# Kernel tuning notes

Hardware: AMD Instinct MI355X
Metric: run time of the kernel (lower is better)

Reference implementation:

```python
import jax, jax.numpy as jnp
import numpy as np

B = 128
K = 16
# (in_ch, featdim, dim) per stage, matching conv1..conv11
DIMS = [(3, 8, 2048), (8, 32, 1024), (32, 64, 512), (64, 64, 256), (64, 64, 128),
        (64, 128, 64), (128, 256, 32), (256, 512, 16), (512, 512, 8), (512, 512, 4),
        (512, 1024, 2)]


def setup_inputs() -> dict:
    key = jax.random.key(0)
    ks = jax.random.split(key, 64)
    inp = {"x": jax.random.normal(ks[0], (B, 3, 2048), dtype=jnp.float32)}
    i = 1
    for li, (cin, cf, d) in enumerate(DIMS, start=1):
        inp[f"W{li}"] = jax.random.normal(ks[i], (3 * cf, cin), dtype=jnp.float32) / np.sqrt(cin).astype(np.float32); i += 1
        inp[f"b{li}"] = jax.random.normal(ks[i], (3 * cf,), dtype=jnp.float32) * 0.01; i += 1
        inp[f"sel{li}"] = jax.random.randint(ks[i], (d,), 0, 3); i += 1
    inp["fcW"] = jax.random.normal(ks[i], (K, 1024), dtype=jnp.float32) / np.sqrt(1024).astype(np.float32); i += 1
    inp["fcb"] = jax.random.normal(ks[i], (K,), dtype=jnp.float32) * 0.01
    return inp


def kdconv(x, W, b, sel, featdim, dim):
    # 1x1 conv == per-position matmul: x [B, Cin, dim] -> y [B, 3*featdim, dim]
    y = jax.nn.relu(jnp.einsum('oi,bin->bon', W, x) + b[None, :, None])
    y = y.reshape(-1, featdim, 3, dim)
    # kd split-dim gather: pick one of the 3 feature groups per position
    y = jnp.take_along_axis(y, sel[None, None, None, :], axis=2)[:, :, 0, :]  # [B, featdim, dim]
    # pairwise max-pool of sibling leaves
    return y.reshape(-1, featdim, dim // 2, 2).max(axis=-1)  # [B, featdim, dim//2]


def reference(x, sel1, sel2, sel3, sel4, sel5, sel6, sel7, sel8, sel9, sel10, sel11,
              W1, b1, W2, b2, W3, b3, W4, b4, W5, b5, W6, b6, W7, b7, W8, b8,
              W9, b9, W10, b10, W11, b11, fcW, fcb):
    Ws = [W1, W2, W3, W4, W5, W6, W7, W8, W9, W10, W11]
    bs = [b1, b2, b3, b4, b5, b6, b7, b8, b9, b10, b11]
    sels = [sel1, sel2, sel3, sel4, sel5, sel6, sel7, sel8, sel9, sel10, sel11]
    h = x
    for (cin, cf, d), W, b, s in zip(DIMS, Ws, bs, sels):
        h = kdconv(h, W, b, s, cf, d)
    h = h.reshape(-1, 1024)  # [B, 1024]
    return jax.nn.log_softmax(h @ fcW.T + fcb, axis=-1)
```

## Files before the change

### kernel.cpp

```cpp
#include <hip/hip_runtime.h>
#include <math.h>

typedef __attribute__((ext_vector_type(8))) short bf16x8;
typedef __attribute__((ext_vector_type(4))) float f32x4;

__device__ __forceinline__ unsigned short f2bf(float f) {
    unsigned u = __builtin_bit_cast(unsigned, f);
    u += 0x7FFF + ((u >> 16) & 1);
    return (unsigned short)(u >> 16);
}
__device__ __forceinline__ float bf2f(unsigned short h) {
    unsigned u = ((unsigned)h) << 16;
    return __builtin_bit_cast(float, u);
}

#define O_W3 0
#define O_W4 6144
#define O_W5 18432
#define O_W6 30720
#define O_W7 55296
#define O_W8 153600
#define O_W9 546816
#define O_W10 1333248
#define O_W11 2119680

template<int CIN>
__device__ __forceinline__ void mfma_tile(
    const unsigned short* a0, const unsigned short* a1,
    const unsigned short* b0p, const unsigned short* b1p,
    f32x4& acc0, f32x4& acc1)
{
#pragma unroll
    for (int k = 0; k < CIN; k += 32) {
        bf16x8 A0 = __builtin_bit_cast(bf16x8, *(const float4*)(const void*)(a0 + k));
        bf16x8 A1 = __builtin_bit_cast(bf16x8, *(const float4*)(const void*)(a1 + k));
        bf16x8 B0 = __builtin_bit_cast(bf16x8, *(const float4*)(const void*)(b0p + k));
        bf16x8 B1 = __builtin_bit_cast(bf16x8, *(const float4*)(const void*)(b1p + k));
        acc0 = __builtin_amdgcn_mfma_f32_16x16x32_bf16(A0, B0, acc0, 0, 0, 0);
        acc1 = __builtin_amdgcn_mfma_f32_16x16x32_bf16(A1, B1, acc1, 0, 0, 0);
    }
}

__device__ __forceinline__ void epilogue_store(
    unsigned short* dst, const f32x4& acc0, const f32x4& acc1,
    const float* bias, int fbase, int s0, int s1)
{
    unsigned short o[4];
#pragma unroll
    for (int r = 0; r < 4; ++r) {
        float v = fmaxf(fmaxf(acc0[r] + bias[(fbase + r) * 3 + s0],
                              acc1[r] + bias[(fbase + r) * 3 + s1]), 0.f);
        o[r] = f2bf(v);
    }
    *(ushort4*)dst = make_ushort4(o[0], o[1], o[2], o[3]);
}

struct PackParams { const float* Wsrc[9]; unsigned short* Wb; };

__global__ __launch_bounds__(256) void pack_w_kernel(PackParams P)
{
    int gt = blockIdx.x * 256 + threadIdx.x;
    const int we[9] = {6144, 12288, 12288, 24576, 98304, 393216, 786432, 786432, 1572864};
    int off = 0;
#pragma unroll
    for (int li = 0; li < 9; ++li) {
        const float4* src = (const float4*)P.Wsrc[li];
        ushort4* dst = (ushort4*)(P.Wb + off);
        int n4 = we[li] >> 2;
        for (int i = gt; i < n4; i += 65536) {
            float4 w = src[i];
            dst[i] = make_ushort4(f2bf(w.x), f2bf(w.y), f2bf(w.z), f2bf(w.w));
        }
        off += we[li];
    }
}

struct FusedParams {
    const float* x;
    const float* W1; const float* B1; const int* S1;
    const float* W2; const float* B2; const int* S2;
    const float* Bl[9];
    const int*   Sl[9];
    const unsigned short* Wb;
    unsigned short* X8;
};

#define A_XS   0
#define A_L1O  25344
#define A_WSM  41728
#define A_L2O  45568
#define A_L3O  0
#define A_L4O  45568
#define A_L5O  0
#define A_L6O  45568
#define ARENA_BYTES 86528

__global__ __launch_bounds__(512) void fused17_kernel(FusedParams P)
{
    __shared__ __align__(16) char arena[ARENA_BYTES];

    const int tid  = threadIdx.x;
    const int bg   = blockIdx.x >> 4;
    const int sl   = blockIdx.x & 15;
    const int lane = tid & 63;
    const int wv   = tid >> 6;
    const int c    = lane & 15, q = lane >> 4;

    const unsigned short* W3b = P.Wb + O_W3;
    const unsigned short* W4b = P.Wb + O_W4;
    const unsigned short* W5b = P.Wb + O_W5;
    const unsigned short* W6b = P.Wb + O_W6;
    const unsigned short* W7b = P.Wb + O_W7;

    {
        float* xsf = (float*)(arena + A_XS);
        const float* xg = P.x + (size_t)(bg * 16) * 6144 + sl * 128;
        for (int i = tid; i < 6144; i += 512) {
            int b = i / 384;
            int r = i - b * 384;
            int cc = r >> 7, p = r & 127;
            xsf[b * 396 + cc * 132 + p] = xg[(size_t)b * 6144 + cc * 2048 + p];
        }
        float* wsm = (float*)(arena + A_WSM);
        for (int i = tid; i < 960; i += 512) {
            float v;
            if (i < 72)       v = P.W1[i];
            else if (i < 96)  v = P.B1[i - 72];
            else if (i < 864) v = P.W2[i - 96];
            else              v = P.B2[i - 864];
            wsm[i] = v;
        }
    }
    __syncthreads();

    {
        const float* xsf = (const float*)(arena + A_XS);
        const float* wl1 = (const float*)(arena + A_WSM);
        const float* bl1 = wl1 + 72;
        unsigned short* L1o = (unsigned short*)(arena + A_L1O);
        for (int i = tid; i < 1024; i += 512) {
            int n = i >> 4, b = i & 15;
            int np1 = sl * 64 + n;
            int s0 = P.S1[2 * np1], s1 = P.S1[2 * np1 + 1];
            const float* xb0 = xsf + b * 396 + 2 * n;
            float c0x = xb0[0],   c0y = xb0[1];
            float c1x = xb0[132], c1y = xb0[133];
            float c2x = xb0[264], c2y = xb0[265];
            unsigned short o[8];
#pragma unroll
            for (int f = 0; f < 8; ++f) {
                int r0 = f * 3 + s0, r1 = f * 3 + s1;
                float z0 = fmaf(wl1[r0*3+2], c2x, fmaf(wl1[r0*3+1], c1x, fmaf(wl1[r0*3+0], c0x, bl1[r0])));
                float z1 = fmaf(wl1[r1*3+2], c2y, fmaf(wl1[r1*3+1], c1y, fmaf(wl1[r1*3+0], c0y, bl1[r1])));
                o[f] = f2bf(fmaxf(fmaxf(z0, z1), 0.f));
            }
            unsigned short* dst = L1o + (n * 16 + b) * 8;
            *(ushort4*)dst       = make_ushort4(o[0], o[1], o[2], o[3]);
            *(ushort4*)(dst + 4) = make_ushort4(o[4], o[5], o[6], o[7]);
        }
    }
    __syncthreads();

    {
        const float* wl2 = (const float*)(arena + A_WSM) + 96;
        const float* bl2 = (const float*)(arena + A_WSM) + 864;
        const unsigned short* L1o = (const unsigned short*)(arena + A_L1O);
        unsigned short* L2o = (unsigned short*)(arena + A_L2O);
        {
            int i = tid;
            int n = i >> 4, b = i & 15;
            int np2 = sl * 32 + n;
            int s0 = P.S2[2 * np2], s1 = P.S2[2 * np2 + 1];
            const unsigned short* r0 = L1o + ((2 * n) * 16 + b) * 8;
            const unsigned short* r1 = L1o + ((2 * n + 1) * 16 + b) * 8;
            float xa[8], xb2[8];
            {
                ushort4 u0 = *(const ushort4*)r0, u1 = *(const ushort4*)(r0 + 4);
                ushort4 v0 = *(const ushort4*)r1, v1 = *(const ushort4*)(r1 + 4);
                xa[0]=bf2f(u0.x); xa[1]=bf2f(u0.y); xa[2]=bf2f(u0.z); xa[3]=bf2f(u0.w);
                xa[4]=bf2f(u1.x); xa[5]=bf2f(u1.y); xa[6]=bf2f(u1.z); xa[7]=bf2f(u1.w);
                xb2[0]=bf2f(v0.x); xb2[1]=bf2f(v0.y); xb2[2]=bf2f(v0.z); xb2[3]=bf2f(v0.w);
                xb2[4]=bf2f(v1.x); xb2[5]=bf2f(v1.y); xb2[6]=bf2f(v1.z); xb2[7]=bf2f(v1.w);
            }
            unsigned short o[32];
#pragma unroll
            for (int f = 0; f < 32; ++f) {
                const float* w0 = &wl2[(f * 3 + s0) * 8];
                const float* w1 = &wl2[(f * 3 + s1) * 8];
                float z0 = bl2[f * 3 + s0], z1 = bl2[f * 3 + s1];
#pragma unroll
                for (int k = 0; k < 8; ++k) {
                    z0 = fmaf(w0[k], xa[k], z0);
                    z1 = fmaf(w1[k], xb2[k], z1);
                }
                o[f] = f2bf(fmaxf(fmaxf(z0, z1), 0.f));
            }
            unsigned short* dst = L2o + (n * 16 + b) * 40;
#pragma unroll
            for (int i2 = 0; i2 < 8; ++i2)
                *(ushort4*)(dst + 4 * i2) = make_ushort4(o[4*i2], o[4*i2+1], o[4*i2+2], o[4*i2+3]);
        }
    }
    __syncthreads();

    {
        const unsigned short* L2o = (const unsigned short*)(arena + A_L2O);
        unsigned short* L3o = (unsigned short*)(arena + A_L3O);
        const int* S3 = P.Sl[0]; const float* B3 = P.Bl[0];
#pragma unroll 2
        for (int t = wv; t < 64; t += 8) {
            int n3 = t >> 2, ft = t & 3;
            int np = sl * 16 + n3;
            int s0 = __builtin_amdgcn_readfirstlane(S3[2 * np]);
            int s1 = __builtin_amdgcn_readfirstlane(S3[2 * np + 1]);
            int f0 = ft * 16;
            const unsigned short* a0 = W3b + ((f0 + c) * 3 + s0) * 32 + q * 8;
            const unsigned short* a1 = W3b + ((f0 + c) * 3 + s1) * 32 + q * 8;
            const unsigned short* bp0 = L2o + ((2 * n3) * 16 + c) * 40 + q * 8;
            const unsigned short* bp1 = L2o + ((2 * n3 + 1) * 16 + c) * 40 + q * 8;
            f32x4 acc0 = {0.f,0.f,0.f,0.f}, acc1 = {0.f,0.f,0.f,0.f};
            mfma_tile<32>(a0, a1, bp0, bp1, acc0, acc1);
            epilogue_store(L3o + (n3 * 16 + c) * 72 + f0 + q * 4,
                           acc0, acc1, B3, f0 + q * 4, s0, s1);
        }
    }
    __syncthreads();

    {
        const unsigned short* L3o = (const unsigned short*)(arena + A_L3O);
        unsigned short* L4o = (unsigned short*)(arena + A_L4O);
        const int* S4 = P.Sl[1]; const float* B4 = P.Bl[1];
#pragma unroll 2
        for (int t = wv; t < 32; t += 8) {
            int n4 = t >> 2, ft = t & 3;
            int np = sl * 8 + n4;
            int s0 = __builtin_amdgcn_readfirstlane(S4[2 * np]);
            int s1 = __builtin_amdgcn_readfirstlane(S4[2 * np + 1]);
            int f0 = ft * 16;
            const unsigned short* a0 = W4b + ((f0 + c) * 3 + s0) * 64 + q * 8;
            const unsigned short* a1 = W4b + ((f0 + c) * 3 + s1) * 64 + q * 8;
            const unsigned short* bp0 = L3o + ((2 * n4) * 16 + c) * 72 + q * 8;
            const unsigned short* bp1 = L3o + ((2 * n4 + 1) * 16 + c) * 72 + q * 8;
            f32x4 acc0 = {0.f,0.f,0.f,0.f}, acc1 = {0.f,0.f,0.f,0.f};
            mfma_tile<64>(a0, a1, bp0, bp1, acc0, acc1);
            epilogue_store(L4o + (n4 * 16 + c) * 72 + f0 + q * 4,
                           acc0, acc1, B4, f0 + q * 4, s0, s1);
        }
    }
    __syncthreads();

    {
        const unsigned short* L4o = (const unsigned short*)(arena + A_L4O);
        unsigned short* L5o = (unsigned short*)(arena + A_L5O);
        const int* S5 = P.Sl[2]; const float* B5 = P.Bl[2];
        for (int t = wv; t < 16; t += 8) {
            int n5 = t >> 2, ft = t & 3;
            int np = sl * 4 + n5;
            int s0 = __builtin_amdgcn_readfirstlane(S5[2 * np]);
            int s1 = __builtin_amdgcn_readfirstlane(S5[2 * np + 1]);
            int f0 = ft * 16;
            const unsigned short* a0 = W5b + ((f0 + c) * 3 + s0) * 64 + q * 8;
            const unsigned short* a1 = W5b + ((f0 + c) * 3 + s1) * 64 + q * 8;
            const unsigned short* bp0 = L4o + ((2 * n5) * 16 + c) * 72 + q * 8;
            const unsigned short* bp1 = L4o + ((2 * n5 + 1) * 16 + c) * 72 + q * 8;
            f32x4 acc0 = {0.f,0.f,0.f,0.f}, acc1 = {0.f,0.f,0.f,0.f};
            mfma_tile<64>(a0, a1, bp0, bp1, acc0, acc1);
            epilogue_store(L5o + (n5 * 16 + c) * 72 + f0 + q * 4,
                           acc0, acc1, B5, f0 + q * 4, s0, s1);
        }
    }
    __syncthreads();

    {
        const unsigned short* L5o = (const unsigned short*)(arena + A_L5O);
        unsigned short* L6o = (unsigned short*)(arena + A_L6O);
        const int* S6 = P.Sl[3]; const float* B6 = P.Bl[3];
        for (int t = wv; t < 16; t += 8) {
            int n6 = t >> 3, ft = t & 7;
            int np = sl * 2 + n6;
            int s0 = __builtin_amdgcn_readfirstlane(S6[2 * np]);
            int s1 = __builtin_amdgcn_readfirstlane(S6[2 * np + 1]);
            int f0 = ft * 16;
            const unsigned short* a0 = W6b + ((f0 + c) * 3 + s0) * 64 + q * 8;
            const unsigned short* a1 = W6b + ((f0 + c) * 3 + s1) * 64 + q * 8;
            const unsigned short* bp0 = L5o + ((2 * n6) * 16 + c) * 72 + q * 8;
            const unsigned short* bp1 = L5o + ((2 * n6 + 1) * 16 + c) * 72 + q * 8;
            f32x4 acc0 = {0.f,0.f,0.f,0.f}, acc1 = {0.f,0.f,0.f,0.f};
            mfma_tile<64>(a0, a1, bp0, bp1, acc0, acc1);
            epilogue_store(L6o + (n6 * 16 + c) * 136 + f0 + q * 4,
                           acc0, acc1, B6, f0 + q * 4, s0, s1);
        }
    }
    __syncthreads();

    {
        const unsigned short* L6o = (const unsigned short*)(arena + A_L6O);
        const int* S7 = P.Sl[4]; const float* B7 = P.Bl[4];
        int s0 = __builtin_amdgcn_readfirstlane(S7[2 * sl]);
        int s1 = __builtin_amdgcn_readfirstlane(S7[2 * sl + 1]);
#pragma unroll 2
        for (int t = wv; t < 16; t += 8) {
            int f0 = t * 16;
            const unsigned short* a0 = W7b + (size_t)((f0 + c) * 3 + s0) * 128 + q * 8;
            const unsigned short* a1 = W7b + (size_t)((f0 + c) * 3 + s1) * 128 + q * 8;
            const unsigned short* bp0 = L6o + (0 * 16 + c) * 136 + q * 8;
            const unsigned short* bp1 = L6o + (1 * 16 + c) * 136 + q * 8;
            f32x4 acc0 = {0.f,0.f,0.f,0.f}, acc1 = {0.f,0.f,0.f,0.f};
            mfma_tile<128>(a0, a1, bp0, bp1, acc0, acc1);
            epilogue_store(P.X8 + ((size_t)sl * 128 + bg * 16 + c) * 256 + f0 + q * 4,
                           acc0, acc1, B7, f0 + q * 4, s0, s1);
        }
    }
}

template<int CIN, int CF, int NP, int MW, int NW>
__global__ __launch_bounds__(256) void mfma_kernel(
    const unsigned short* __restrict__ Xin,
    const unsigned short* __restrict__ Wb,
    const float* __restrict__ bias,
    const int*   __restrict__ sel,
    unsigned short* __restrict__ Xout)
{
    constexpr int FT = CF / (16 * MW);
    constexpr int BT = 128 / (16 * NW);

    const int wid  = threadIdx.x >> 6;
    const int lane = threadIdx.x & 63;
    const int task = blockIdx.x * 4 + wid;
    const int bi = task % BT;
    const int fi = (task / BT) % FT;
    const int n  = task / (BT * FT);

    const int c = lane & 15;
    const int q = lane >> 4;
    const int s0 = __builtin_amdgcn_readfirstlane(sel[2 * n]);
    const int s1 = __builtin_amdgcn_readfirstlane(sel[2 * n + 1]);

    const int f0 = fi * 16 * MW;
    const int b0 = bi * 16 * NW;

    const unsigned short* ap[2][MW];
    const unsigned short* bp[2][NW];
#pragma unroll
    for (int p = 0; p < 2; ++p) {
        int s = p ? s1 : s0;
#pragma unroll
        for (int mi = 0; mi < MW; ++mi)
            ap[p][mi] = Wb + (size_t)((f0 + mi * 16 + c) * 3 + s) * CIN + q * 8;
#pragma unroll
        for (int ni = 0; ni < NW; ++ni)
            bp[p][ni] = Xin + ((size_t)(2 * n + p) * 128 + b0 + ni * 16 + c) * CIN + q * 8;
    }

    f32x4 acc[2][MW][NW];
#pragma unroll
    for (int p = 0; p < 2; ++p)
#pragma unroll
        for (int mi = 0; mi < MW; ++mi)
#pragma unroll
            for (int ni = 0; ni < NW; ++ni)
                acc[p][mi][ni] = (f32x4){0.f, 0.f, 0.f, 0.f};

#pragma unroll 2
    for (int k = 0; k < CIN; k += 32) {
        bf16x8 A[2][MW], B[2][NW];
#pragma unroll
        for (int p = 0; p < 2; ++p) {
#pragma unroll
            for (int mi = 0; mi < MW; ++mi)
                A[p][mi] = __builtin_bit_cast(bf16x8, *(const float4*)(const void*)(ap[p][mi] + k));
#pragma unroll
            for (int ni = 0; ni < NW; ++ni)
                B[p][ni] = __builtin_bit_cast(bf16x8, *(const float4*)(const void*)(bp[p][ni] + k));
        }
#pragma unroll
        for (int p = 0; p < 2; ++p)
#pragma unroll
            for (int mi = 0; mi < MW; ++mi)
#pragma unroll
                for (int ni = 0; ni < NW; ++ni)
                    acc[p][mi][ni] = __builtin_amdgcn_mfma_f32_16x16x32_bf16(
                        A[p][mi], B[p][ni], acc[p][mi][ni], 0, 0, 0);
    }

#pragma unroll
    for (int mi = 0; mi < MW; ++mi) {
        int fbase = f0 + mi * 16 + q * 4;
#pragma unroll
        for (int ni = 0; ni < NW; ++ni) {
            int b = b0 + ni * 16 + c;
            epilogue_store(Xout + ((size_t)n * 128 + b) * CF + fbase,
                           acc[0][mi][ni], acc[1][mi][ni], bias, fbase, s0, s1);
        }
    }
}

__global__ __launch_bounds__(256) void fc_logsoftmax_kernel(
    const unsigned short* __restrict__ h, const float* __restrict__ fcW,
    const float* __restrict__ fcb, float* __restrict__ out)
{
    int b   = blockIdx.x;
    int tid = threadIdx.x;
    int k     = tid & 15;
    int chunk = tid >> 4;

    const float* __restrict__ wk = fcW + (size_t)k * 1024;
    const unsigned short* hb = h + (size_t)b * 1024;

    float partial = 0.0f;
    int j0 = chunk * 64;
#pragma unroll 8
    for (int j = 0; j < 64; ++j)
        partial = fmaf(bf2f(hb[j0 + j]), wk[j0 + j], partial);

    __shared__ float red[16][17];
    red[chunk][k] = partial;
    __syncthreads();

    __shared__ float logits[16];
    if (tid < 16) {
        float s = fcb[tid];
#pragma unroll
        for (int c = 0; c < 16; ++c) s += red[c][tid];
        logits[tid] = s;
    }
    __syncthreads();

    if (tid < 16) {
        float mx = -INFINITY;
#pragma unroll
        for (int kk = 0; kk < 16; ++kk) mx = fmaxf(mx, logits[kk]);
        float se = 0.0f;
#pragma unroll
        for (int kk = 0; kk < 16; ++kk) se += expf(logits[kk] - mx);
        out[b * 16 + tid] = logits[tid] - mx - logf(se);
    }
}

extern "C" void kernel_launch(void* const* d_in, const int* in_sizes, int n_in,
                              void* d_out, int out_size, void* d_ws, size_t ws_size,
                              hipStream_t stream)
{
#define WL(i) (const float*)d_in[1 + 3 * (i)]
#define BL(i) (const float*)d_in[2 + 3 * (i)]
#define SL(i) (const int*)  d_in[3 + 3 * (i)]

    unsigned short* bufA = (unsigned short*)d_ws;
    unsigned short* bufB = bufA + 2u * 1024u * 1024u;
    unsigned short* Wb   = bufB + 2u * 1024u * 1024u;

    PackParams PP;
    for (int i = 0; i < 9; ++i) PP.Wsrc[i] = WL(2 + i);
    PP.Wb = Wb;
    pack_w_kernel<<<256, 256, 0, stream>>>(PP);

    FusedParams FP;
    FP.x  = (const float*)d_in[0];
    FP.W1 = WL(0); FP.B1 = BL(0); FP.S1 = SL(0);
    FP.W2 = WL(1); FP.B2 = BL(1); FP.S2 = SL(1);
    for (int i = 0; i < 9; ++i) {
        FP.Bl[i] = BL(2 + i);
        FP.Sl[i] = SL(2 + i);
    }
    FP.Wb = Wb; FP.X8 = bufA;
    fused17_kernel<<<128, 512, 0, stream>>>(FP);

    mfma_kernel<256, 512, 8, 2, 2><<<128, 256, 0, stream>>>(bufA, Wb + O_W8,  BL(7),  SL(7),  bufB);
    mfma_kernel<512, 512, 4, 1, 1><<<256, 256, 0, stream>>>(bufB, Wb + O_W9,  BL(8),  SL(8),  bufA);
    mfma_kernel<512, 512, 2, 1, 1><<<128, 256, 0, stream>>>(bufA, Wb + O_W10, BL(9),  SL(9),  bufB);
    mfma_kernel<512, 1024, 1, 1, 1><<<128, 256, 0, stream>>>(bufB, Wb + O_W11, BL(10), SL(10), bufA);

    fc_logsoftmax_kernel<<<128, 256, 0, stream>>>(bufA, (const float*)d_in[34], (const float*)d_in[35], (float*)d_out);

#undef WL
#undef BL
#undef SL
}
```

Baseline: 211.6 us.

## Fold weight packing into fused kernel and read early-layer weights as fp32

Removes the separate pack_w kernel launch. Extra blocks of the fused layer-1..7 kernel now convert the W8–W11 weights to bf16, running alongside the 128 compute blocks. Layers 3–7 read fp32 weights directly and convert them in registers instead of waiting for packed copies. The fused kernel also grows to 1024 threads per block, stages selection indices and biases in shared memory, and drops its per-stage loops. This saves a launch and a serialization point, at the cost of redundant per-block fp32→bf16 conversion and twice the weight bytes read for layers 3–7.

```diff
diff --git a/kernel.cpp b/kernel.cpp
--- a/kernel.cpp
+++ b/kernel.cpp
@@ -14,26 +14,32 @@
     return __builtin_bit_cast(float, u);
 }
 
-#define O_W3 0
-#define O_W4 6144
-#define O_W5 18432
-#define O_W6 30720
-#define O_W7 55296
 #define O_W8 153600
 #define O_W9 546816
 #define O_W10 1333248
 #define O_W11 2119680
 
+__device__ __forceinline__ bf16x8 ldcvt8(const float* p) {
+    float4 u0 = *(const float4*)p;
+    float4 u1 = *(const float4*)(p + 4);
+    bf16x8 r;
+    r[0] = (short)f2bf(u0.x); r[1] = (short)f2bf(u0.y);
+    r[2] = (short)f2bf(u0.z); r[3] = (short)f2bf(u0.w);
+    r[4] = (short)f2bf(u1.x); r[5] = (short)f2bf(u1.y);
+    r[6] = (short)f2bf(u1.z); r[7] = (short)f2bf(u1.w);
+    return r;
+}
+
 template<int CIN>
-__device__ __forceinline__ void mfma_tile(
-    const unsigned short* a0, const unsigned short* a1,
+__device__ __forceinline__ void mfma_tile_f32A(
+    const float* a0f, const float* a1f,
     const unsigned short* b0p, const unsigned short* b1p,
     f32x4& acc0, f32x4& acc1)
 {
 #pragma unroll
     for (int k = 0; k < CIN; k += 32) {
-        bf16x8 A0 = __builtin_bit_cast(bf16x8, *(const float4*)(const void*)(a0 + k));
-        bf16x8 A1 = __builtin_bit_cast(bf16x8, *(const float4*)(const void*)(a1 + k));
+        bf16x8 A0 = ldcvt8(a0f + k);
+        bf16x8 A1 = ldcvt8(a1f + k);
         bf16x8 B0 = __builtin_bit_cast(bf16x8, *(const float4*)(const void*)(b0p + k));
         bf16x8 B1 = __builtin_bit_cast(bf16x8, *(const float4*)(const void*)(b1p + k));
         acc0 = __builtin_amdgcn_mfma_f32_16x16x32_bf16(A0, B0, acc0, 0, 0, 0);
@@ -55,80 +61,105 @@
     *(ushort4*)dst = make_ushort4(o[0], o[1], o[2], o[3]);
 }
 
-struct PackParams { const float* Wsrc[9]; unsigned short* Wb; };
-
-__global__ __launch_bounds__(256) void pack_w_kernel(PackParams P)
-{
-    int gt = blockIdx.x * 256 + threadIdx.x;
-    const int we[9] = {6144, 12288, 12288, 24576, 98304, 393216, 786432, 786432, 1572864};
-    int off = 0;
-#pragma unroll
-    for (int li = 0; li < 9; ++li) {
-        const float4* src = (const float4*)P.Wsrc[li];
-        ushort4* dst = (ushort4*)(P.Wb + off);
-        int n4 = we[li] >> 2;
-        for (int i = gt; i < n4; i += 65536) {
-            float4 w = src[i];
-            dst[i] = make_ushort4(f2bf(w.x), f2bf(w.y), f2bf(w.z), f2bf(w.w));
-        }
-        off += we[li];
-    }
-}
-
 struct FusedParams {
     const float* x;
     const float* W1; const float* B1; const int* S1;
     const float* W2; const float* B2; const int* S2;
+    const float* Wsrc[9];
     const float* Bl[9];
     const int*   Sl[9];
-    const unsigned short* Wb;
+    unsigned short* Wb;
     unsigned short* X8;
 };
 
-#define A_XS   0
-#define A_L1O  25344
-#define A_WSM  41728
-#define A_L2O  45568
-#define A_L3O  0
-#define A_L4O  45568
-#define A_L5O  0
-#define A_L6O  45568
-#define ARENA_BYTES 86528
-
-__global__ __launch_bounds__(512) void fused17_kernel(FusedParams P)
-{
+#define A_SELB 0
+#define A_XS   8192
+#define A_L1O  33536
+#define A_WSM  49920
+#define A_L2O  53760
+#define A_L3O  8192
+#define A_L4O  53760
+#define A_L5O  8192
+#define A_L6O  53760
+#define ARENA_BYTES 94720
+
+__global__ __launch_bounds__(1024) void fused17_kernel(FusedParams P)
+{
+    const int tid = threadIdx.x;
+
+    if (blockIdx.x >= 128) {
+        int gt = (blockIdx.x - 128) * 1024 + tid;
+        const int we[4] = {393216, 786432, 786432, 1572864};
+        const int wo[4] = {O_W8, O_W9, O_W10, O_W11};
+#pragma unroll
+        for (int li = 0; li < 4; ++li) {
+            const float4* src = (const float4*)P.Wsrc[5 + li];
+            ushort4* dst = (ushort4*)(P.Wb + wo[li]);
+            int n4 = we[li] >> 2;
+            for (int i = gt; i < n4; i += 65536) {
+                float4 w = src[i];
+                dst[i] = make_ushort4(f2bf(w.x), f2bf(w.y), f2bf(w.z), f2bf(w.w));
+            }
+        }
+        return;
+    }
+
     __shared__ __align__(16) char arena[ARENA_BYTES];
 
-    const int tid  = threadIdx.x;
     const int bg   = blockIdx.x >> 4;
     const int sl   = blockIdx.x & 15;
     const int lane = tid & 63;
     const int wv   = tid >> 6;
     const int c    = lane & 15, q = lane >> 4;
 
-    const unsigned short* W3b = P.Wb + O_W3;
-    const unsigned short* W4b = P.Wb + O_W4;
-    const unsigned short* W5b = P.Wb + O_W5;
-    const unsigned short* W6b = P.Wb + O_W6;
-    const unsigned short* W7b = P.Wb + O_W7;
+    int*   si  = (int*)(arena + A_SELB);
+    float* bfs = (float*)(arena + A_SELB + 1024);
+    const int* S1L = si;
+    const int* S2L = si + 128;
+    const int* S3L = si + 192;
+    const int* S4L = si + 224;
+    const int* S5L = si + 240;
+    const int* S6L = si + 248;
+    const int* S7L = si + 252;
+    const float* B3L = bfs;
+    const float* B4L = bfs + 192;
+    const float* B5L = bfs + 384;
+    const float* B6L = bfs + 576;
+    const float* B7L = bfs + 960;
 
     {
         float* xsf = (float*)(arena + A_XS);
         const float* xg = P.x + (size_t)(bg * 16) * 6144 + sl * 128;
-        for (int i = tid; i < 6144; i += 512) {
+        for (int i = tid; i < 6144; i += 1024) {
             int b = i / 384;
             int r = i - b * 384;
             int cc = r >> 7, p = r & 127;
             xsf[b * 396 + cc * 132 + p] = xg[(size_t)b * 6144 + cc * 2048 + p];
         }
         float* wsm = (float*)(arena + A_WSM);
-        for (int i = tid; i < 960; i += 512) {
+        if (tid < 960) {
             float v;
-            if (i < 72)       v = P.W1[i];
-            else if (i < 96)  v = P.B1[i - 72];
-            else if (i < 864) v = P.W2[i - 96];
-            else              v = P.B2[i - 864];
-            wsm[i] = v;
+            if (tid < 72)       v = P.W1[tid];
+            else if (tid < 96)  v = P.B1[tid - 72];
+            else if (tid < 864) v = P.W2[tid - 96];
+            else                v = P.B2[tid - 864];
+            wsm[tid] = v;
+        }
+        if (tid < 128)      si[tid] = P.S1[sl * 128 + tid];
+        else if (tid < 192) si[tid] = P.S2[sl * 64 + (tid - 128)];
+        else if (tid < 224) si[tid] = P.Sl[0][sl * 32 + (tid - 192)];
+        else if (tid < 240) si[tid] = P.Sl[1][sl * 16 + (tid - 224)];
+        else if (tid < 248) si[tid] = P.Sl[2][sl * 8  + (tid - 240)];
+        else if (tid < 252) si[tid] = P.Sl[3][sl * 4  + (tid - 248)];
+        else if (tid < 254) si[tid] = P.Sl[4][sl * 2  + (tid - 252)];
+        for (int i = tid; i < 1728; i += 1024) {
+            float v;
+            if (i < 192)      v = P.Bl[0][i];
+            else if (i < 384) v = P.Bl[1][i - 192];
+            else if (i < 576) v = P.Bl[2][i - 384];
+            else if (i < 960) v = P.Bl[3][i - 576];
+            else              v = P.Bl[4][i - 960];
+            bfs[i] = v;
         }
     }
     __syncthreads();
@@ -138,26 +169,23 @@
         const float* wl1 = (const float*)(arena + A_WSM);
         const float* bl1 = wl1 + 72;
         unsigned short* L1o = (unsigned short*)(arena + A_L1O);
-        for (int i = tid; i < 1024; i += 512) {
-            int n = i >> 4, b = i & 15;
-            int np1 = sl * 64 + n;
-            int s0 = P.S1[2 * np1], s1 = P.S1[2 * np1 + 1];
-            const float* xb0 = xsf + b * 396 + 2 * n;
-            float c0x = xb0[0],   c0y = xb0[1];
-            float c1x = xb0[132], c1y = xb0[133];
-            float c2x = xb0[264], c2y = xb0[265];
-            unsigned short o[8];
-#pragma unroll
-            for (int f = 0; f < 8; ++f) {
-                int r0 = f * 3 + s0, r1 = f * 3 + s1;
-                float z0 = fmaf(wl1[r0*3+2], c2x, fmaf(wl1[r0*3+1], c1x, fmaf(wl1[r0*3+0], c0x, bl1[r0])));
-                float z1 = fmaf(wl1[r1*3+2], c2y, fmaf(wl1[r1*3+1], c1y, fmaf(wl1[r1*3+0], c0y, bl1[r1])));
-                o[f] = f2bf(fmaxf(fmaxf(z0, z1), 0.f));
-            }
-            unsigned short* dst = L1o + (n * 16 + b) * 8;
-            *(ushort4*)dst       = make_ushort4(o[0], o[1], o[2], o[3]);
-            *(ushort4*)(dst + 4) = make_ushort4(o[4], o[5], o[6], o[7]);
-        }
+        int n = tid >> 4, b = tid & 15;
+        int s0 = S1L[2 * n], s1 = S1L[2 * n + 1];
+        const float* xb0 = xsf + b * 396 + 2 * n;
+        float c0x = xb0[0],   c0y = xb0[1];
+        float c1x = xb0[132], c1y = xb0[133];
+        float c2x = xb0[264], c2y = xb0[265];
+        unsigned short o[8];
+#pragma unroll
+        for (int f = 0; f < 8; ++f) {
+            int r0 = f * 3 + s0, r1 = f * 3 + s1;
+            float z0 = fmaf(wl1[r0*3+2], c2x, fmaf(wl1[r0*3+1], c1x, fmaf(wl1[r0*3+0], c0x, bl1[r0])));
+            float z1 = fmaf(wl1[r1*3+2], c2y, fmaf(wl1[r1*3+1], c1y, fmaf(wl1[r1*3+0], c0y, bl1[r1])));
+            o[f] = f2bf(fmaxf(fmaxf(z0, z1), 0.f));
+        }
+        unsigned short* dst = L1o + (n * 16 + b) * 8;
+        *(ushort4*)dst       = make_ushort4(o[0], o[1], o[2], o[3]);
+        *(ushort4*)(dst + 4) = make_ushort4(o[4], o[5], o[6], o[7]);
     }
     __syncthreads();
 
@@ -166,62 +194,58 @@
         const float* bl2 = (const float*)(arena + A_WSM) + 864;
         const unsigned short* L1o = (const unsigned short*)(arena + A_L1O);
         unsigned short* L2o = (unsigned short*)(arena + A_L2O);
+        int n = tid >> 5, b = (tid >> 1) & 15, fh = tid & 1;
+        int s0 = S2L[2 * n], s1 = S2L[2 * n + 1];
+        const unsigned short* r0 = L1o + ((2 * n) * 16 + b) * 8;
+        const unsigned short* r1 = L1o + ((2 * n + 1) * 16 + b) * 8;
+        float xa[8], xb2[8];
         {
-            int i = tid;
-            int n = i >> 4, b = i & 15;
-            int np2 = sl * 32 + n;
-            int s0 = P.S2[2 * np2], s1 = P.S2[2 * np2 + 1];
-            const unsigned short* r0 = L1o + ((2 * n) * 16 + b) * 8;
-            const unsigned short* r1 = L1o + ((2 * n + 1) * 16 + b) * 8;
-            float xa[8], xb2[8];
-            {
-                ushort4 u0 = *(const ushort4*)r0, u1 = *(const ushort4*)(r0 + 4);
-                ushort4 v0 = *(const ushort4*)r1, v1 = *(const ushort4*)(r1 + 4);
-                xa[0]=bf2f(u0.x); xa[1]=bf2f(u0.y); xa[2]=bf2f(u0.z); xa[3]=bf2f(u0.w);
-                xa[4]=bf2f(u1.x); xa[5]=bf2f(u1.y); xa[6]=bf2f(u1.z); xa[7]=bf2f(u1.w);
-                xb2[0]=bf2f(v0.x); xb2[1]=bf2f(v0.y); xb2[2]=bf2f(v0.z); xb2[3]=bf2f(v0.w);
-                xb2[4]=bf2f(v1.x); xb2[5]=bf2f(v1.y); xb2[6]=bf2f(v1.z); xb2[7]=bf2f(v1.w);
+            ushort4 u0 = *(const ushort4*)r0, u1 = *(const ushort4*)(r0 + 4);
+            ushort4 v0 = *(const ushort4*)r1, v1 = *(const ushort4*)(r1 + 4);
+            xa[0]=bf2f(u0.x); xa[1]=bf2f(u0.y); xa[2]=bf2f(u0.z); xa[3]=bf2f(u0.w);
+            xa[4]=bf2f(u1.x); xa[5]=bf2f(u1.y); xa[6]=bf2f(u1.z); xa[7]=bf2f(u1.w);
+            xb2[0]=bf2f(v0.x); xb2[1]=bf2f(v0.y); xb2[2]=bf2f(v0.z); xb2[3]=bf2f(v0.w);
+            xb2[4]=bf2f(v1.x); xb2[5]=bf2f(v1.y); xb2[6]=bf2f(v1.z); xb2[7]=bf2f(v1.w);
+        }
+        unsigned short o[16];
+#pragma unroll
+        for (int fl = 0; fl < 16; ++fl) {
+            int f = fh * 16 + fl;
+            const float* w0 = &wl2[(f * 3 + s0) * 8];
+            const float* w1 = &wl2[(f * 3 + s1) * 8];
+            float z0 = bl2[f * 3 + s0], z1 = bl2[f * 3 + s1];
+#pragma unroll
+            for (int k = 0; k < 8; ++k) {
+                z0 = fmaf(w0[k], xa[k], z0);
+                z1 = fmaf(w1[k], xb2[k], z1);
             }
-            unsigned short o[32];
-#pragma unroll
-            for (int f = 0; f < 32; ++f) {
-                const float* w0 = &wl2[(f * 3 + s0) * 8];
-                const float* w1 = &wl2[(f * 3 + s1) * 8];
-                float z0 = bl2[f * 3 + s0], z1 = bl2[f * 3 + s1];
-#pragma unroll
-                for (int k = 0; k < 8; ++k) {
-                    z0 = fmaf(w0[k], xa[k], z0);
-                    z1 = fmaf(w1[k], xb2[k], z1);
-                }
-                o[f] = f2bf(fmaxf(fmaxf(z0, z1), 0.f));
-            }
-            unsigned short* dst = L2o + (n * 16 + b) * 40;
-#pragma unroll
-            for (int i2 = 0; i2 < 8; ++i2)
-                *(ushort4*)(dst + 4 * i2) = make_ushort4(o[4*i2], o[4*i2+1], o[4*i2+2], o[4*i2+3]);
-        }
+            o[fl] = f2bf(fmaxf(fmaxf(z0, z1), 0.f));
+        }
+        unsigned short* dst = L2o + (n * 16 + b) * 40 + fh * 16;
+#pragma unroll
+        for (int i2 = 0; i2 < 4; ++i2)
+            *(ushort4*)(dst + 4 * i2) = make_ushort4(o[4*i2], o[4*i2+1], o[4*i2+2], o[4*i2+3]);
     }
     __syncthreads();
 
     {
         const unsigned short* L2o = (const unsigned short*)(arena + A_L2O);
         unsigned short* L3o = (unsigned short*)(arena + A_L3O);
-        const int* S3 = P.Sl[0]; const float* B3 = P.Bl[0];
+        const float* W3f = P.Wsrc[0];
 #pragma unroll 2
-        for (int t = wv; t < 64; t += 8) {
+        for (int t = wv; t < 64; t += 16) {
             int n3 = t >> 2, ft = t & 3;
-            int np = sl * 16 + n3;
-            int s0 = __builtin_amdgcn_readfirstlane(S3[2 * np]);
-            int s1 = __builtin_amdgcn_readfirstlane(S3[2 * np + 1]);
+            int s0 = __builtin_amdgcn_readfirstlane(S3L[2 * n3]);
+            int s1 = __builtin_amdgcn_readfirstlane(S3L[2 * n3 + 1]);
             int f0 = ft * 16;
-            const unsigned short* a0 = W3b + ((f0 + c) * 3 + s0) * 32 + q * 8;
-            const unsigned short* a1 = W3b + ((f0 + c) * 3 + s1) * 32 + q * 8;
+            const float* a0f = W3f + ((f0 + c) * 3 + s0) * 32 + q * 8;
+            const float* a1f = W3f + ((f0 + c) * 3 + s1) * 32 + q * 8;
             const unsigned short* bp0 = L2o + ((2 * n3) * 16 + c) * 40 + q * 8;
             const unsigned short* bp1 = L2o + ((2 * n3 + 1) * 16 + c) * 40 + q * 8;
             f32x4 acc0 = {0.f,0.f,0.f,0.f}, acc1 = {0.f,0.f,0.f,0.f};
-            mfma_tile<32>(a0, a1, bp0, bp1, acc0, acc1);
+            mfma_tile_f32A<32>(a0f, a1f, bp0, bp1, acc0, acc1);
             epilogue_store(L3o + (n3 * 16 + c) * 72 + f0 + q * 4,
-                           acc0, acc1, B3, f0 + q * 4, s0, s1);
+                           acc0, acc1, B3L, f0 + q * 4, s0, s1);
         }
     }
     __syncthreads();
@@ -229,22 +253,21 @@
     {
         const unsigned short* L3o = (const unsigned short*)(arena + A_L3O);
         unsigned short* L4o = (unsigned short*)(arena + A_L4O);
-        const int* S4 = P.Sl[1]; const float* B4 = P.Bl[1];
-#pragma unroll 2
-        for (int t = wv; t < 32; t += 8) {
+        const float* W4f = P.Wsrc[1];
+#pragma unroll
+        for (int t = wv; t < 32; t += 16) {
             int n4 = t >> 2, ft = t & 3;
-            int np = sl * 8 + n4;
-            int s0 = __builtin_amdgcn_readfirstlane(S4[2 * np]);
-            int s1 = __builtin_amdgcn_readfirstlane(S4[2 * np + 1]);
+            int s0 = __builtin_amdgcn_readfirstlane(S4L[2 * n4]);
+            int s1 = __builtin_amdgcn_readfirstlane(S4L[2 * n4 + 1]);
             int f0 = ft * 16;
-            const unsigned short* a0 = W4b + ((f0 + c) * 3 + s0) * 64 + q * 8;
-            const unsigned short* a1 = W4b + ((f0 + c) * 3 + s1) * 64 + q * 8;
+            const float* a0f = W4f + ((f0 + c) * 3 + s0) * 64 + q * 8;
+            const float* a1f = W4f + ((f0 + c) * 3 + s1) * 64 + q * 8;
             const unsigned short* bp0 = L3o + ((2 * n4) * 16 + c) * 72 + q * 8;
             const unsigned short* bp1 = L3o + ((2 * n4 + 1) * 16 + c) * 72 + q * 8;
             f32x4 acc0 = {0.f,0.f,0.f,0.f}, acc1 = {0.f,0.f,0.f,0.f};
-            mfma_tile<64>(a0, a1, bp0, bp1, acc0, acc1);
+            mfma_tile_f32A<64>(a0f, a1f, bp0, bp1, acc0, acc1);
             epilogue_store(L4o + (n4 * 16 + c) * 72 + f0 + q * 4,
-                           acc0, acc1, B4, f0 + q * 4, s0, s1);
+                           acc0, acc1, B4L, f0 + q * 4, s0, s1);
         }
     }
     __syncthreads();
@@ -252,64 +275,57 @@
     {
         const unsigned short* L4o = (const unsigned short*)(arena + A_L4O);
         unsigned short* L5o = (unsigned short*)(arena + A_L5O);
-        const int* S5 = P.Sl[2]; const float* B5 = P.Bl[2];
-        for (int t = wv; t < 16; t += 8) {
-            int n5 = t >> 2, ft = t & 3;
-            int np = sl * 4 + n5;
-            int s0 = __builtin_amdgcn_readfirstlane(S5[2 * np]);
-            int s1 = __builtin_amdgcn_readfirstlane(S5[2 * np + 1]);
-            int f0 = ft * 16;
-            const unsigned short* a0 = W5b + ((f0 + c) * 3 + s0) * 64 + q * 8;
-            const unsigned short* a1 = W5b + ((f0 + c) * 3 + s1) * 64 + q * 8;
-            const unsigned short* bp0 = L4o + ((2 * n5) * 16 + c) * 72 + q * 8;
-            const unsigned short* bp1 = L4o + ((2 * n5 + 1) * 16 + c) * 72 + q * 8;
-            f32x4 acc0 = {0.f,0.f,0.f,0.f}, acc1 = {0.f,0.f,0.f,0.f};
-            mfma_tile<64>(a0, a1, bp0, bp1, acc0, acc1);
-            epilogue_store(L5o + (n5 * 16 + c) * 72 + f0 + q * 4,
-                           acc0, acc1, B5, f0 + q * 4, s0, s1);
-        }
+        const float* W5f = P.Wsrc[2];
+        int t = wv;
+        int n5 = t >> 2, ft = t & 3;
+        int s0 = __builtin_amdgcn_readfirstlane(S5L[2 * n5]);
+        int s1 = __builtin_amdgcn_readfirstlane(S5L[2 * n5 + 1]);
+        int f0 = ft * 16;
+        const float* a0f = W5f + ((f0 + c) * 3 + s0) * 64 + q * 8;
+        const float* a1f = W5f + ((f0 + c) * 3 + s1) * 64 + q * 8;
+        const unsigned short* bp0 = L4o + ((2 * n5) * 16 + c) * 72 + q * 8;
+        const unsigned short* bp1 = L4o + ((2 * n5 + 1) * 16 + c) * 72 + q * 8;
+        f32x4 acc0 = {0.f,0.f,0.f,0.f}, acc1 = {0.f,0.f,0.f,0.f};
+        mfma_tile_f32A<64>(a0f, a1f, bp0, bp1, acc0, acc1);
+        epilogue_store(L5o + (n5 * 16 + c) * 72 + f0 + q * 4,
+                       acc0, acc1, B5L, f0 + q * 4, s0, s1);
     }
     __syncthreads();
 
     {
         const unsigned short* L5o = (const unsigned short*)(arena + A_L5O);
         unsigned short* L6o = (unsigned short*)(arena + A_L6O);
-        const int* S6 = P.Sl[3]; const float* B6 = P.Bl[3];
-        for (int t = wv; t < 16; t += 8) {
-            int n6 = t >> 3, ft = t & 7;
-            int np = sl * 2 + n6;
-            int s0 = __builtin_amdgcn_readfirstlane(S6[2 * np]);
-            int s1 = __builtin_amdgcn_readfirstlane(S6[2 * np + 1]);
-            int f0 = ft * 16;
-            const unsigned short* a0 = W6b + ((f0 + c) * 3 + s0) * 64 + q * 8;
-            const unsigned short* a1 = W6b + ((f0 + c) * 3 + s1) * 64 + q * 8;
-            const unsigned short* bp0 = L5o + ((2 * n6) * 16 + c) * 72 + q * 8;
-            const unsigned short* bp1 = L5o + ((2 * n6 + 1) * 16 + c) * 72 + q * 8;
-            f32x4 acc0 = {0.f,0.f,0.f,0.f}, acc1 = {0.f,0.f,0.f,0.f};
-            mfma_tile<64>(a0, a1, bp0, bp1, acc0, acc1);
-            epilogue_store(L6o + (n6 * 16 + c) * 136 + f0 + q * 4,
-                           acc0, acc1, B6, f0 + q * 4, s0, s1);
-        }
+        const float* W6f = P.Wsrc[3];
+        int t = wv;
+        int n6 = t >> 3, ft = t & 7;
+        int s0 = __builtin_amdgcn_readfirstlane(S6L[2 * n6]);
+        int s1 = __builtin_amdgcn_readfirstlane(S6L[2 * n6 + 1]);
+        int f0 = ft * 16;
+        const float* a0f = W6f + ((f0 + c) * 3 + s0) * 64 + q * 8;
+        const float* a1f = W6f + ((f0 + c) * 3 + s1) * 64 + q * 8;
+        const unsigned short* bp0 = L5o + ((2 * n6) * 16 + c) * 72 + q * 8;
+        const unsigned short* bp1 = L5o + ((2 * n6 + 1) * 16 + c) * 72 + q * 8;
+        f32x4 acc0 = {0.f,0.f,0.f,0.f}, acc1 = {0.f,0.f,0.f,0.f};
+        mfma_tile_f32A<64>(a0f, a1f, bp0, bp1, acc0, acc1);
+        epilogue_store(L6o + (n6 * 16 + c) * 136 + f0 + q * 4,
+                       acc0, acc1, B6L, f0 + q * 4, s0, s1);
     }
     __syncthreads();
 
     {
         const unsigned short* L6o = (const unsigned short*)(arena + A_L6O);
-        const int* S7 = P.Sl[4]; const float* B7 = P.Bl[4];
-        int s0 = __builtin_amdgcn_readfirstlane(S7[2 * sl]);
-        int s1 = __builtin_amdgcn_readfirstlane(S7[2 * sl + 1]);
-#pragma unroll 2
-        for (int t = wv; t < 16; t += 8) {
-            int f0 = t * 16;
-            const unsigned short* a0 = W7b + (size_t)((f0 + c) * 3 + s0) * 128 + q * 8;
-            const unsigned short* a1 = W7b + (size_t)((f0 + c) * 3 + s1) * 128 + q * 8;
-            const unsigned short* bp0 = L6o + (0 * 16 + c) * 136 + q * 8;
-            const unsigned short* bp1 = L6o + (1 * 16 + c) * 136 + q * 8;
-            f32x4 acc0 = {0.f,0.f,0.f,0.f}, acc1 = {0.f,0.f,0.f,0.f};
-            mfma_tile<128>(a0, a1, bp0, bp1, acc0, acc1);
-            epilogue_store(P.X8 + ((size_t)sl * 128 + bg * 16 + c) * 256 + f0 + q * 4,
-                           acc0, acc1, B7, f0 + q * 4, s0, s1);
-        }
+        const float* W7f = P.Wsrc[4];
+        int s0 = __builtin_amdgcn_readfirstlane(S7L[0]);
+        int s1 = __builtin_amdgcn_readfirstlane(S7L[1]);
+        int f0 = wv * 16;
+        const float* a0f = W7f + (size_t)((f0 + c) * 3 + s0) * 128 + q * 8;
+        const float* a1f = W7f + (size_t)((f0 + c) * 3 + s1) * 128 + q * 8;
+        const unsigned short* bp0 = L6o + (0 * 16 + c) * 136 + q * 8;
+        const unsigned short* bp1 = L6o + (1 * 16 + c) * 136 + q * 8;
+        f32x4 acc0 = {0.f,0.f,0.f,0.f}, acc1 = {0.f,0.f,0.f,0.f};
+        mfma_tile_f32A<128>(a0f, a1f, bp0, bp1, acc0, acc1);
+        epilogue_store(P.X8 + ((size_t)sl * 128 + bg * 16 + c) * 256 + f0 + q * 4,
+                       acc0, acc1, B7L, f0 + q * 4, s0, s1);
     }
 }
 
@@ -449,21 +465,17 @@
     unsigned short* bufB = bufA + 2u * 1024u * 1024u;
     unsigned short* Wb   = bufB + 2u * 1024u * 1024u;
 
-    PackParams PP;
-    for (int i = 0; i < 9; ++i) PP.Wsrc[i] = WL(2 + i);
-    PP.Wb = Wb;
-    pack_w_kernel<<<256, 256, 0, stream>>>(PP);
-
     FusedParams FP;
     FP.x  = (const float*)d_in[0];
     FP.W1 = WL(0); FP.B1 = BL(0); FP.S1 = SL(0);
     FP.W2 = WL(1); FP.B2 = BL(1); FP.S2 = SL(1);
     for (int i = 0; i < 9; ++i) {
-        FP.Bl[i] = BL(2 + i);
-        FP.Sl[i] = SL(2 + i);
+        FP.Wsrc[i] = WL(2 + i);
+        FP.Bl[i]   = BL(2 + i);
+        FP.Sl[i]   = SL(2 + i);
     }
     FP.Wb = Wb; FP.X8 = bufA;
-    fused17_kernel<<<128, 512, 0, stream>>>(FP);
+    fused17_kernel<<<192, 1024, 0, stream>>>(FP);
 
     mfma_kernel<256, 512, 8, 2, 2><<<128, 256, 0, stream>>>(bufA, Wb + O_W8,  BL(7),  SL(7),  bufB);
     mfma_kernel<512, 512, 4, 1, 1><<<256, 256, 0, stream>>>(bufB, Wb + O_W9,  BL(8),  SL(8),  bufA);
```

Result: no change. 215.0 us (+1.6%).
